# Kernel tuning notes

Hardware: AMD Instinct MI355X
Metric: run time of the kernel (lower is better)

The kernel has to match this reference:

```python
import jax, jax.numpy as jnp
import numpy as np

BATCH_SIZE = 4096
DIM = 128
TEMPERATURE = 0.5
EPS = 1e-8


def setup_inputs() -> dict:
    key = jax.random.key(0)
    k1, k2 = jax.random.split(key)
    z_i = jax.random.normal(k1, (BATCH_SIZE, DIM), dtype=jnp.float32)
    z_j = jax.random.normal(k2, (BATCH_SIZE, DIM), dtype=jnp.float32)
    return {"z_i": z_i, "z_j": z_j}


def reference(z_i, z_j):
    B = z_i.shape[0]
    N = 2 * B
    z = jnp.concatenate([z_i, z_j], axis=0)  # [N, D]
    # cosine similarity = matmul of L2-normalized rows (avoids the NxNxD broadcast)
    zn = z / jnp.maximum(jnp.linalg.norm(z, axis=1, keepdims=True), EPS)
    sim = (zn @ zn.T) / TEMPERATURE  # [N, N]
    idx = jnp.arange(N)
    # positive pair: row i pairs with row (i+B) mod N (covers both diag offsets +B and -B)
    pos = sim[idx, (idx + B) % N]  # [N]
    # CE over logits [pos, negatives]; the logit set per row is the full sim row
    # minus the self-similarity (diagonal). Mask diagonal with a large negative.
    neg_inf = jnp.asarray(-1e9, sim.dtype)
    sim_masked = jnp.where(idx[:, None] == idx[None, :], neg_inf, sim)
    lse = jax.nn.logsumexp(sim_masked, axis=1)  # [N]
    # CrossEntropyLoss(reduction='sum') with label 0 (the positive), divided by N
    loss = jnp.sum(lse - pos) / N
    return loss
```

## Files before the change

kernel.cpp:

```cpp
#include <hip/hip_runtime.h>
#include <cstdint>


#define BROWS 4096
#define NROWS 8192
#define ROWB  256
#define CSPL  24
#define CT32  256
#define BRT   256
#define TILEB 8192

typedef __attribute__((ext_vector_type(8))) __bf16    bf16x8;
typedef __attribute__((ext_vector_type(4))) float     f32x4;
typedef __attribute__((ext_vector_type(4))) uint32_t  u32x4;

#define K1F 2.8853900817779268f
#define LN2F 0.69314718055994531f
#define BC8(x) __builtin_bit_cast(bf16x8, x)

__device__ __forceinline__ uint16_t f2bf(float f) {
    uint32_t u = __builtin_bit_cast(uint32_t, f);
    u = (u + 0x7FFFu + ((u >> 16) & 1u)) >> 16;
    return (uint16_t)u;
}
__device__ __forceinline__ float bf2f(uint16_t b) {
    return __builtin_bit_cast(float, ((uint32_t)b) << 16);
}
__device__ __forceinline__ void gload_lds16(const void* g, void* l) {
    __builtin_amdgcn_global_load_lds(
        (const __attribute__((address_space(1))) void*)g,
        (__attribute__((address_space(3))) void*)l, 16, 0, 0);
}

__global__ __launch_bounds__(256) void k_normalize(
    const float* __restrict__ zi, const float* __restrict__ zj,
    uint16_t* __restrict__ znA, uint16_t* __restrict__ znB)
{
    int tid  = threadIdx.x;
    int lane = tid & 63;
    int wid  = tid >> 6;
    int li   = lane & 7;
    int row  = blockIdx.x * 32 + wid * 8 + (lane >> 3);

    const float* src = (row < BROWS) ? (zi + (size_t)row * 128)
                                     : (zj + (size_t)(row - BROWS) * 128);
    float4 v[4];
    const float4* s4 = (const float4*)(src + li * 16);
#pragma unroll
    for (int c = 0; c < 4; ++c) v[c] = s4[c];

    float ss = 0.f;
#pragma unroll
    for (int c = 0; c < 4; ++c)
        ss += v[c].x*v[c].x + v[c].y*v[c].y + v[c].z*v[c].z + v[c].w*v[c].w;
#pragma unroll
    for (int off = 1; off < 8; off <<= 1) ss += __shfl_xor(ss, off);

    float scale = 1.0f / fmaxf(sqrtf(ss), 1e-8f);

    float e[16];
#pragma unroll
    for (int c = 0; c < 4; ++c) {
        e[c*4+0] = v[c].x * scale; e[c*4+1] = v[c].y * scale;
        e[c*4+2] = v[c].z * scale; e[c*4+3] = v[c].w * scale;
    }
    uint32_t wB[8], wA[8];
#pragma unroll
    for (int q = 0; q < 8; ++q) {
        wB[q] = (uint32_t)f2bf(e[2*q])       | ((uint32_t)f2bf(e[2*q+1])       << 16);
        wA[q] = (uint32_t)f2bf(e[2*q] * K1F) | ((uint32_t)f2bf(e[2*q+1] * K1F) << 16);
    }
    uint4* dB = (uint4*)((char*)znB + (size_t)row * ROWB + li * 32);
    dB[0] = make_uint4(wB[0], wB[1], wB[2], wB[3]);
    dB[1] = make_uint4(wB[4], wB[5], wB[6], wB[7]);
    uint4* dA = (uint4*)((char*)znA + (size_t)row * ROWB + li * 32);
    dA[0] = make_uint4(wA[0], wA[1], wA[2], wA[3]);
    dA[1] = make_uint4(wA[4], wA[5], wA[6], wA[7]);
}

__global__ __launch_bounds__(256)
__attribute__((amdgpu_waves_per_eu(3, 3)))
void k_simlse(
    const uint16_t* __restrict__ znA, const uint16_t* __restrict__ znB,
    float* __restrict__ partial)
{
    __shared__ __align__(16) char lds[3][TILEB];

    const char* zA = (const char*)znA;
    const char* zB = (const char*)znB;
    int tid  = threadIdx.x;
    int lane = tid & 63;
    int wid  = tid >> 6;
    int lo16 = lane & 15;
    int hi4  = lane >> 4;
    int rowBase = blockIdx.x * BRT + wid * 64;

    u32x4 a[4][4];
#pragma unroll
    for (int rt = 0; rt < 4; ++rt) {
        const char* ap = zA + (size_t)(rowBase + rt * 16 + lo16) * ROWB + hi4 * 16;
#pragma unroll
        for (int kf = 0; kf < 4; ++kf)
            a[rt][kf] = *(const u32x4*)(ap + kf * 64);
    }

    float rs[4][4];
#pragma unroll
    for (int rt = 0; rt < 4; ++rt)
#pragma unroll
        for (int r = 0; r < 4; ++r) rs[rt][r] = 0.f;

    int t0 = (CT32 * blockIdx.y) / CSPL;
    int t1 = (CT32 * (blockIdx.y + 1)) / CSPL;
    int nt = t1 - t0;

    const char* gsrc = zB + (size_t)t0 * TILEB
                     + ((tid * 16) ^ (((tid >> 4) & 7) << 4));
    int xorv = (lo16 & 7) << 4;

#define STAGE(sel, t) do {                                                     \
        const char* g_ = gsrc + (size_t)(t) * TILEB;                           \
        gload_lds16(g_,        &lds[sel][wid * 1024]);                         \
        gload_lds16(g_ + 4096, &lds[sel][4096 + wid * 1024]);                  \
    } while (0)

#define COMPUTE(sel) do {                                                        \
        _Pragma("unroll")                                                        \
        for (int ct = 0; ct < 2; ++ct) {                                         \
            const char* lb_ = &lds[sel][ct * 4096 + lo16 * 256];                 \
            u32x4 bf[4];                                                         \
            _Pragma("unroll")                                                    \
            for (int kf = 0; kf < 4; ++kf)                                       \
                bf[kf] = *(const u32x4*)(lb_ + ((hi4 * 16 + kf * 64) ^ xorv));   \
            f32x4 ac0 = {0.f,0.f,0.f,0.f}, ac1 = {0.f,0.f,0.f,0.f};              \
            f32x4 ac2 = {0.f,0.f,0.f,0.f}, ac3 = {0.f,0.f,0.f,0.f};              \
            _Pragma("unroll")                                                    \
            for (int kf = 0; kf < 4; ++kf) {                                     \
                bf16x8 bk_ = BC8(bf[kf]);                                        \
                ac0 = __builtin_amdgcn_mfma_f32_16x16x32_bf16(BC8(a[0][kf]), bk_, ac0, 0, 0, 0); \
                ac1 = __builtin_amdgcn_mfma_f32_16x16x32_bf16(BC8(a[1][kf]), bk_, ac1, 0, 0, 0); \
                ac2 = __builtin_amdgcn_mfma_f32_16x16x32_bf16(BC8(a[2][kf]), bk_, ac2, 0, 0, 0); \
                ac3 = __builtin_amdgcn_mfma_f32_16x16x32_bf16(BC8(a[3][kf]), bk_, ac3, 0, 0, 0); \
            }                                                                    \
            _Pragma("unroll")                                                    \
            for (int r = 0; r < 4; ++r) {                                        \
                rs[0][r] += __builtin_amdgcn_exp2f(ac0[r]);                      \
                rs[1][r] += __builtin_amdgcn_exp2f(ac1[r]);                      \
                rs[2][r] += __builtin_amdgcn_exp2f(ac2[r]);                      \
                rs[3][r] += __builtin_amdgcn_exp2f(ac3[r]);                      \
            }                                                                    \
        }                                                                        \
    } while (0)

    STAGE(0, 0);
    STAGE(1, 1);

    int t = 0;
    for (; t < nt - 1; ++t) {
        asm volatile("s_waitcnt vmcnt(2)" ::: "memory");
        __builtin_amdgcn_s_barrier();
        __builtin_amdgcn_sched_barrier(0);
        COMPUTE(t % 3);
        if (t + 2 < nt) STAGE((t + 2) % 3, t + 2);
    }
    asm volatile("s_waitcnt vmcnt(0)" ::: "memory");
    __builtin_amdgcn_s_barrier();
    __builtin_amdgcn_sched_barrier(0);
    COMPUTE(t % 3);

#undef STAGE
#undef COMPUTE

#pragma unroll
    for (int rt = 0; rt < 4; ++rt)
#pragma unroll
        for (int r = 0; r < 4; ++r) {
            float s = rs[rt][r];
            s += __shfl_xor(s, 1);  s += __shfl_xor(s, 2);
            s += __shfl_xor(s, 4);  s += __shfl_xor(s, 8);
            if (lo16 == 0) {
                int row = rowBase + rt * 16 + hi4 * 4 + r;
                partial[blockIdx.y * NROWS + row] = s;
            }
        }
}

__global__ __launch_bounds__(256) void k_finalize(
    const uint16_t* __restrict__ znA, const uint16_t* __restrict__ znB,
    const float* __restrict__ partial, float* __restrict__ blocksum)
{
    int tid = threadIdx.x;
    int r   = tid >> 3;
    int sub = tid & 7;
    int i = blockIdx.x * 32 + r;

    float S = 0.f;
#pragma unroll
    for (int k = 0; k < 3; ++k) S += partial[(size_t)(sub + k * 8) * NROWS + i];

    int j = (i + BROWS) & (NROWS - 1);
    const uint4* rAi = (const uint4*)((const char*)znA + (size_t)i * ROWB);
    const uint4* rBi = (const uint4*)((const char*)znB + (size_t)i * ROWB);
    const uint4* rBj = (const uint4*)((const char*)znB + (size_t)j * ROWB);
    float adot = 0.f;
    float sdot = 0.f;
#pragma unroll
    for (int cc = 0; cc < 2; ++cc) {
        int c = sub * 2 + cc;
        uint4 ua = rAi[c], ub = rBi[c], vb = rBj[c];
        const uint32_t* pa = (const uint32_t*)&ua;
        const uint32_t* pb = (const uint32_t*)&ub;
        const uint32_t* pv = (const uint32_t*)&vb;
#pragma unroll
        for (int q = 0; q < 4; ++q) {
            float a0 = bf2f((uint16_t)(pa[q] & 0xffffu)), a1 = bf2f((uint16_t)(pa[q] >> 16));
            float b0 = bf2f((uint16_t)(pb[q] & 0xffffu)), b1 = bf2f((uint16_t)(pb[q] >> 16));
            float v0 = bf2f((uint16_t)(pv[q] & 0xffffu)), v1 = bf2f((uint16_t)(pv[q] >> 16));
            adot += a0 * v0 + a1 * v1;
            sdot += a0 * b0 + a1 * b1;
        }
    }
#pragma unroll
    for (int off = 1; off < 8; off <<= 1) {
        S    += __shfl_xor(S, off);
        adot += __shfl_xor(adot, off);
        sdot += __shfl_xor(sdot, off);
    }

    float c = 0.f;
    if (sub == 0) {
        S -= __builtin_amdgcn_exp2f(sdot);
        c = LN2F * (__builtin_amdgcn_logf(S) - adot);
    }
#pragma unroll
    for (int off = 1; off < 64; off <<= 1) c += __shfl_xor(c, off);
    __shared__ float wsum[4];
    int lane = tid & 63, wid = tid >> 6;
    if (lane == 0) wsum[wid] = c;
    __syncthreads();
    if (tid == 0) blocksum[blockIdx.x] = wsum[0] + wsum[1] + wsum[2] + wsum[3];
}

__global__ __launch_bounds__(64) void k_reduce(
    const float* __restrict__ blocksum, float* __restrict__ out)
{
    int tid = threadIdx.x;
    float v = 0.f;
#pragma unroll
    for (int k = 0; k < 4; ++k) v += blocksum[tid + k * 64];
#pragma unroll
    for (int off = 1; off < 64; off <<= 1) v += __shfl_xor(v, off);
    if (tid == 0) out[0] = v * (1.0f / (float)NROWS);
}

extern "C" void kernel_launch(void* const* d_in, const int* in_sizes, int n_in,
                              void* d_out, int out_size, void* d_ws, size_t ws_size,
                              hipStream_t stream)
{
    const float* zi = (const float*)d_in[0];
    const float* zj = (const float*)d_in[1];
    float* out = (float*)d_out;

    char* ws = (char*)d_ws;
    uint16_t* znA      = (uint16_t*)ws;
    uint16_t* znB      = (uint16_t*)(ws + (size_t)NROWS * ROWB);
    float*    partial  = (float*)(ws + 2 * (size_t)NROWS * ROWB);
    float*    blocksum = (float*)(ws + 2 * (size_t)NROWS * ROWB
                                     + (size_t)CSPL * NROWS * 4);

    k_normalize<<<dim3(256), dim3(256), 0, stream>>>(zi, zj, znA, znB);
    k_simlse  <<<dim3(32, CSPL), dim3(256), 0, stream>>>(znA, znB, partial);
    k_finalize<<<dim3(256), dim3(256), 0, stream>>>(znA, znB, partial, blocksum);
    k_reduce  <<<dim3(1), dim3(64), 0, stream>>>(blocksum, out);
}
```

Before: 34.64 us.

## Swizzle simlse block order per XCD and fold final reduce into atomics

The 2D grid of the similarity kernel is flattened to 768 blocks and remapped so consecutive blocks that land on the same XCD (bid&7) share column tiles, which should improve L2 reuse of the B tiles. The separate single-block reduction kernel is removed: finalize blocks atomically add their scaled partial sums into the output, which is zeroed with a memset. This trades one kernel launch for a memset plus 256 float atomics, and makes summation order nondeterministic.

```diff
diff --git a/kernel.cpp b/kernel.cpp
--- a/kernel.cpp
+++ b/kernel.cpp
@@ -93,7 +93,12 @@
     int wid  = tid >> 6;
     int lo16 = lane & 15;
     int hi4  = lane >> 4;
-    int rowBase = blockIdx.x * BRT + wid * 64;
+
+    int bid = blockIdx.x;
+    int swz = (bid & 7) * 96 + (bid >> 3);
+    int bx  = swz & 31;
+    int by  = swz >> 5;
+    int rowBase = bx * BRT + wid * 64;
 
     u32x4 a[4][4];
 #pragma unroll
@@ -110,8 +115,8 @@
 #pragma unroll
         for (int r = 0; r < 4; ++r) rs[rt][r] = 0.f;
 
-    int t0 = (CT32 * blockIdx.y) / CSPL;
-    int t1 = (CT32 * (blockIdx.y + 1)) / CSPL;
+    int t0 = (CT32 * by) / CSPL;
+    int t1 = (CT32 * (by + 1)) / CSPL;
     int nt = t1 - t0;
 
     const char* gsrc = zB + (size_t)t0 * TILEB
@@ -180,14 +185,14 @@
             s += __shfl_xor(s, 4);  s += __shfl_xor(s, 8);
             if (lo16 == 0) {
                 int row = rowBase + rt * 16 + hi4 * 4 + r;
-                partial[blockIdx.y * NROWS + row] = s;
+                partial[(size_t)by * NROWS + row] = s;
             }
         }
 }
 
 __global__ __launch_bounds__(256) void k_finalize(
     const uint16_t* __restrict__ znA, const uint16_t* __restrict__ znB,
-    const float* __restrict__ partial, float* __restrict__ blocksum)
+    const float* __restrict__ partial, float* __restrict__ out)
 {
     int tid = threadIdx.x;
     int r   = tid >> 3;
@@ -238,19 +243,9 @@
     int lane = tid & 63, wid = tid >> 6;
     if (lane == 0) wsum[wid] = c;
     __syncthreads();
-    if (tid == 0) blocksum[blockIdx.x] = wsum[0] + wsum[1] + wsum[2] + wsum[3];
-}
-
-__global__ __launch_bounds__(64) void k_reduce(
-    const float* __restrict__ blocksum, float* __restrict__ out)
-{
-    int tid = threadIdx.x;
-    float v = 0.f;
-#pragma unroll
-    for (int k = 0; k < 4; ++k) v += blocksum[tid + k * 64];
-#pragma unroll
-    for (int off = 1; off < 64; off <<= 1) v += __shfl_xor(v, off);
-    if (tid == 0) out[0] = v * (1.0f / (float)NROWS);
+    if (tid == 0)
+        atomicAdd(out, (wsum[0] + wsum[1] + wsum[2] + wsum[3])
+                         * (1.0f / (float)NROWS));
 }
 
 extern "C" void kernel_launch(void* const* d_in, const int* in_sizes, int n_in,
@@ -265,11 +260,9 @@
     uint16_t* znA      = (uint16_t*)ws;
     uint16_t* znB      = (uint16_t*)(ws + (size_t)NROWS * ROWB);
     float*    partial  = (float*)(ws + 2 * (size_t)NROWS * ROWB);
-    float*    blocksum = (float*)(ws + 2 * (size_t)NROWS * ROWB
-                                     + (size_t)CSPL * NROWS * 4);
-
+
+    hipMemsetAsync(out, 0, sizeof(float), stream);
     k_normalize<<<dim3(256), dim3(256), 0, stream>>>(zi, zj, znA, znB);
-    k_simlse  <<<dim3(32, CSPL), dim3(256), 0, stream>>>(znA, znB, partial);
-    k_finalize<<<dim3(256), dim3(256), 0, stream>>>(znA, znB, partial, blocksum);
-    k_reduce  <<<dim3(1), dim3(64), 0, stream>>>(blocksum, out);
-}
+    k_simlse  <<<dim3(768), dim3(256), 0, stream>>>(znA, znB, partial);
+    k_finalize<<<dim3(256), dim3(256), 0, stream>>>(znA, znB, partial, out);
+}
```

Result: slower. 41.75 us (+20.5%).
